# Kernel tuning notes

Measured on AMD Instinct MI355X. Metric: run time of the kernel, lower is better.

The kernel has to match this reference:

```python
import jax, jax.numpy as jnp
import numpy as np


def _topk_masked_softmax(attn, k):
    # Keep only the top-k entries per row (last dim), softmax over them.
    _, idx = jax.lax.top_k(attn, k)  # [b, nh, C, k]
    mask = jnp.put_along_axis(
        jnp.zeros(attn.shape, dtype=bool), idx, True, axis=-1, inplace=False
    )
    return jax.nn.softmax(jnp.where(mask, attn, -jnp.inf), axis=-1)


def setup_inputs() -> dict:
    key = jax.random.key(0)
    k0, k1, k2, k3, k4 = jax.random.split(key, 5)
    b, nh, C = 8, 8, 512
    attn = jax.random.normal(k0, (b, nh, C, C), dtype=jnp.float32)
    # In the torch module these are Parameters initialized to 0.2; use random
    # positive scalars of similar scale for a non-degenerate baseline.
    w1 = jax.random.uniform(k1, (1,), dtype=jnp.float32)
    w2 = jax.random.uniform(k2, (1,), dtype=jnp.float32)
    w3 = jax.random.uniform(k3, (1,), dtype=jnp.float32)
    w4 = jax.random.uniform(k4, (1,), dtype=jnp.float32)
    return {"attn": attn, "w1": w1, "w2": w2, "w3": w3, "w4": w4}


def reference(attn, w1, w2, w3, w4):
    C = attn.shape[-1]
    a1 = _topk_masked_softmax(attn, int(C / 2))
    a2 = _topk_masked_softmax(attn, int(C * 2 / 3))
    a3 = _topk_masked_softmax(attn, int(C * 3 / 4))
    a4 = _topk_masked_softmax(attn, int(C * 4 / 5))
    return a1 * w1 + a2 * w2 + a3 * w3 + a4 * w4
```

## Files before the change

### kernel.cpp

```cpp
#include <hip/hip_runtime.h>
#include <math.h>

#define ROW_C 512
#define NBIN 2048
#define NPACK (NBIN / 2)


static __device__ __forceinline__ unsigned scan64_add(unsigned v) {
    int x = (int)v;
    x += __builtin_amdgcn_update_dpp(0, x, 0x111, 0xF, 0xF, false);
    x += __builtin_amdgcn_update_dpp(0, x, 0x112, 0xF, 0xF, false);
    x += __builtin_amdgcn_update_dpp(0, x, 0x114, 0xF, 0xE, false);
    x += __builtin_amdgcn_update_dpp(0, x, 0x118, 0xF, 0xC, false);
    x += __builtin_amdgcn_update_dpp(0, x, 0x142, 0xA, 0xF, false);
    x += __builtin_amdgcn_update_dpp(0, x, 0x143, 0xC, 0xF, false);
    return (unsigned)x;
}

static __device__ __forceinline__ unsigned scan16_add(unsigned v) {
    int x = (int)v;
    x += __builtin_amdgcn_update_dpp(0, x, 0x111, 0xF, 0xF, false);
    x += __builtin_amdgcn_update_dpp(0, x, 0x112, 0xF, 0xF, false);
    x += __builtin_amdgcn_update_dpp(0, x, 0x114, 0xF, 0xE, false);
    x += __builtin_amdgcn_update_dpp(0, x, 0x118, 0xF, 0xC, false);
    return (unsigned)x;
}

static __device__ __forceinline__ float wave_fadd_red(float v) {
    float t;
    t = __int_as_float(__builtin_amdgcn_update_dpp(0, __float_as_int(v), 0x111, 0xF, 0xF, false)); v += t;
    t = __int_as_float(__builtin_amdgcn_update_dpp(0, __float_as_int(v), 0x112, 0xF, 0xF, false)); v += t;
    t = __int_as_float(__builtin_amdgcn_update_dpp(0, __float_as_int(v), 0x114, 0xF, 0xE, false)); v += t;
    t = __int_as_float(__builtin_amdgcn_update_dpp(0, __float_as_int(v), 0x118, 0xF, 0xC, false)); v += t;
    t = __int_as_float(__builtin_amdgcn_update_dpp(0, __float_as_int(v), 0x142, 0xA, 0xF, false)); v += t;
    t = __int_as_float(__builtin_amdgcn_update_dpp(0, __float_as_int(v), 0x143, 0xC, 0xF, false)); v += t;
    return __int_as_float(__builtin_amdgcn_readlane(__float_as_int(v), 63));
}

static __device__ __forceinline__ float wave_fmax_red(float v) {
    const int NI = (int)0xFF800000;
    float t;
    t = __int_as_float(__builtin_amdgcn_update_dpp(NI, __float_as_int(v), 0x111, 0xF, 0xF, false)); v = fmaxf(v, t);
    t = __int_as_float(__builtin_amdgcn_update_dpp(NI, __float_as_int(v), 0x112, 0xF, 0xF, false)); v = fmaxf(v, t);
    t = __int_as_float(__builtin_amdgcn_update_dpp(NI, __float_as_int(v), 0x114, 0xF, 0xE, false)); v = fmaxf(v, t);
    t = __int_as_float(__builtin_amdgcn_update_dpp(NI, __float_as_int(v), 0x118, 0xF, 0xC, false)); v = fmaxf(v, t);
    t = __int_as_float(__builtin_amdgcn_update_dpp(NI, __float_as_int(v), 0x142, 0xA, 0xF, false)); v = fmaxf(v, t);
    t = __int_as_float(__builtin_amdgcn_update_dpp(NI, __float_as_int(v), 0x143, 0xC, 0xF, false)); v = fmaxf(v, t);
    return __int_as_float(__builtin_amdgcn_readlane(__float_as_int(v), 63));
}

__global__ __launch_bounds__(256) void topk_ms_kernel(
    const float* __restrict__ attn,
    const float* __restrict__ w1p, const float* __restrict__ w2p,
    const float* __restrict__ w3p, const float* __restrict__ w4p,
    float* __restrict__ out)
{
    __shared__ __align__(16) unsigned hist_all[4][NPACK];

    const int lane = threadIdx.x & 63;
    const int wv   = threadIdx.x >> 6;
    unsigned* h = hist_all[wv];
    int4* hv = (int4*)h;

    const long long gid   = (long long)blockIdx.x * 4 + wv;
    const long long baseA = gid * (2 * ROW_C) + lane * 8;
    const long long baseB = baseA + ROW_C;

    float xA[8], xB[8];
    {
        const float4 A0 = *reinterpret_cast<const float4*>(attn + baseA);
        const float4 A1 = *reinterpret_cast<const float4*>(attn + baseA + 4);
        const float4 B0 = *reinterpret_cast<const float4*>(attn + baseB);
        const float4 B1 = *reinterpret_cast<const float4*>(attn + baseB + 4);
        xA[0]=A0.x; xA[1]=A0.y; xA[2]=A0.z; xA[3]=A0.w;
        xA[4]=A1.x; xA[5]=A1.y; xA[6]=A1.z; xA[7]=A1.w;
        xB[0]=B0.x; xB[1]=B0.y; xB[2]=B0.z; xB[3]=B0.w;
        xB[4]=B1.x; xB[5]=B1.y; xB[6]=B1.z; xB[7]=B1.w;
    }

    const float NINF = -__builtin_inff();

    auto BINF = [](float v) -> int {
        const float y = __builtin_amdgcn_fmed3f(v, -3.90625f, 3.90625f) + 12.0f;
        return (int)((__float_as_uint(y) >> 12) & 0x7FFu);
    };

    auto ZERO = [&]() {
        const int4 z = make_int4(0, 0, 0, 0);
        hv[lane] = z; hv[lane + 64] = z; hv[lane + 128] = z; hv[lane + 192] = z;
    };

    auto HIST = [&](const float* x) {
        #pragma unroll
        for (int s = 0; s < 8; ++s) {
            const int b  = BINF(x[s]);
            const int j  = b >> 1;
            const int ph = j ^ ((j >> 3) & 0x1C);
            atomicAdd(&h[ph], (b & 1) ? 0x10000u : 1u);
        }
    };

    auto FRONT = [&](float* tthr, int* b_, int* R_, int* al_) {
        unsigned ps = 0;
        #pragma unroll
        for (int k = 0; k < 4; ++k) {
            const int b  = 4 * lane + k;
            const int pb = b ^ ((b >> 3) & 7);
            const int4 v = hv[pb];
            ps += (unsigned)v.x + (unsigned)v.y + (unsigned)v.z + (unsigned)v.w;
        }
        const unsigned tot  = (ps & 0xFFFFu) + (ps >> 16);
        const unsigned incl = scan64_add(tot);
        const unsigned excl = incl - tot;

        const unsigned long long Ba = __ballot(incl >= 257u);
        const unsigned long long Bb = __ballot(incl >= 172u);
        const unsigned long long Bc = __ballot(incl >= 129u);
        const unsigned long long Bd = __ballot(incl >= 104u);
        const int l0 = __ffsll(Ba) - 1, l1 = __ffsll(Bb) - 1,
                  l2 = __ffsll(Bc) - 1, l3 = __ffsll(Bd) - 1;

        const int r = lane >> 4;
        const int lsel = (r == 0) ? l0 : (r == 1) ? l1 : (r == 2) ? l2 : l3;
        const int Tr   = (r == 0) ? 257 : (r == 1) ? 172 : (r == 2) ? 129 : 104;
        const int Kr   = (r == 0) ? 256 : (r == 1) ? 341 : (r == 2) ? 384 : 409;
        const unsigned exl = __shfl(excl, lsel, 64);

        const int jw = (lsel << 4) + (lane & 15);
        const int pw = jw ^ ((jw >> 3) & 0x1C);
        const unsigned w0 = h[pw];
        const unsigned q  = w0 + (w0 << 16);
        const unsigned wt = q >> 16;
        const unsigned sc = scan16_add(wt);
        const unsigned ebase = exl + (sc - wt);
        const int      phi   = (int)(ebase + wt);
        const unsigned long long CB = __ballot(phi >= Tr);
        const int js = __ffs((unsigned)(CB >> (r << 4))) - 1;
        const unsigned q_w  = __shfl(q, (r << 4) + js, 64);
        const unsigned eb_w = __shfl(ebase, (r << 4) + js, 64);

        const int  plo  = (int)(eb_w + (q_w & 0xFFFFu));
        const int  phw  = (int)(eb_w + (q_w >> 16));
        const bool ev   = (plo >= Tr);
        const int  bsel = (((lsel << 4) + js) << 1) + (ev ? 0 : 1);
        const int  locp = ev ? plo : phw;
        const int  prvp = ev ? (int)eb_w : plo;
        const int  Rr   = Kr - 512 + locp;
        const int  alin = (prvp == Tr - 1) ? 1 : 0;
        const unsigned pk = ((unsigned)bsel << 11) | ((unsigned)alin << 10) | (unsigned)Rr;

        const unsigned v0 = (unsigned)__builtin_amdgcn_readlane((int)pk, 0);
        const unsigned v1 = (unsigned)__builtin_amdgcn_readlane((int)pk, 16);
        const unsigned v2 = (unsigned)__builtin_amdgcn_readlane((int)pk, 32);
        const unsigned v3 = (unsigned)__builtin_amdgcn_readlane((int)pk, 48);
        const unsigned vv[4] = {v0, v1, v2, v3};
        #pragma unroll
        for (int rr = 0; rr < 4; ++rr) {
            b_[rr]  = (int)(vv[rr] >> 11);
            al_[rr] = (int)((vv[rr] >> 10) & 1u);
            R_[rr]  = (int)(vv[rr] & 0x3FFu);
            float t = __uint_as_float((unsigned)(b_[rr] + 0x41000) << 12) - 12.0f;
            tthr[rr] = (b_[rr] <= 24) ? NINF : t;
        }
    };

    auto BACK = [&](const float* x, float* tthr, const int* b_, const int* R_,
                    const int* al_, long long obase) {
        int needv[4] = {0,0,0,0}, cntv[4] = {0,0,0,0};
        bool anytb = false;
        const bool needbins = !(al_[0] && al_[1] && al_[2] && al_[3]);
        int bn[8];
        if (needbins) {
            #pragma unroll
            for (int s = 0; s < 8; ++s) bn[s] = BINF(x[s]);
        }
        #pragma unroll
        for (int rr = 0; rr < 4; ++rr) {
            if (!al_[rr]) {
                float cm[8];
                #pragma unroll
                for (int s = 0; s < 8; ++s)
                    cm[s] = (bn[s] == b_[rr]) ? x[s] : NINF;
                int R = R_[rr];
                float t; int c;
                while (true) {
                    float mk = cm[0];
                    #pragma unroll
                    for (int s = 1; s < 8; ++s) mk = fmaxf(mk, cm[s]);
                    t = wave_fmax_red(mk);
                    c = 0;
                    #pragma unroll
                    for (int s = 0; s < 8; ++s)
                        c += (int)__popcll(__ballot(cm[s] == t));
                    if (c >= R) break;
                    R -= c;
                    #pragma unroll
                    for (int s = 0; s < 8; ++s)
                        cm[s] = (cm[s] == t) ? NINF : cm[s];
                }
                tthr[rr] = t; needv[rr] = R; cntv[rr] = c;
                anytb = anytb || (c != R);
            }
        }

        float eo[8];
        #pragma unroll
        for (int s = 0; s < 8; ++s) eo[s] = __expf(x[s]);

        float res[8];
        if (!anytb) {
            const float t1 = tthr[0], t2 = tthr[1], t3 = tthr[2], t4 = tthr[3];
            float z0 = 0.f, z1 = 0.f, z2 = 0.f, z3 = 0.f;
            #pragma unroll
            for (int s = 0; s < 8; ++s) {
                z0 += (x[s] >= t1) ? eo[s] : 0.f;
                z1 += (x[s] >= t2) ? eo[s] : 0.f;
                z2 += (x[s] >= t3) ? eo[s] : 0.f;
                z3 += (x[s] >= t4) ? eo[s] : 0.f;
            }
            const float Z0 = wave_fadd_red(z0);
            const float Z1 = wave_fadd_red(z1);
            const float Z2 = wave_fadd_red(z2);
            const float Z3 = wave_fadd_red(z3);
            const float wz0 = w1p[0] * __builtin_amdgcn_rcpf(Z0);
            const float wz1 = w2p[0] * __builtin_amdgcn_rcpf(Z1);
            const float wz2 = w3p[0] * __builtin_amdgcn_rcpf(Z2);
            const float wz3 = w4p[0] * __builtin_amdgcn_rcpf(Z3);
            const float u4 = wz3, u3 = u4 + wz2, u2 = u3 + wz1, u1 = u2 + wz0;
            #pragma unroll
            for (int s = 0; s < 8; ++s) {
                float c = (x[s] >= t1) ? u1 : u2;
                c = (x[s] >= t2) ? c : u3;
                c = (x[s] >= t3) ? c : u4;
                c = (x[s] >= t4) ? c : 0.f;
                res[s] = eo[s] * c;
            }
        } else {
            int fl[8] = {0, 0, 0, 0, 0, 0, 0, 0};
            #pragma unroll
            for (int rr = 0; rr < 4; ++rr) {
                const float t = tthr[rr];
                if (al_[rr] || needv[rr] == cntv[rr]) {
                    #pragma unroll
                    for (int s = 0; s < 8; ++s)
                        fl[s] |= ((int)(x[s] >= t)) << rr;
                } else {
                    const unsigned long long ltm = (1ull << lane) - 1ull;
                    int basec = 0;
                    #pragma unroll
                    for (int s = 0; s < 8; ++s)
                        basec += (int)__popcll(__ballot(x[s] == t) & ltm);
                    int own = 0;
                    #pragma unroll
                    for (int s = 0; s < 8; ++s) {
                        const bool eq = (x[s] == t);
                        if (x[s] > t || (eq && (basec + own) < needv[rr]))
                            fl[s] |= (1 << rr);
                        own += eq ? 1 : 0;
                    }
                }
            }
            float z0 = 0.f, z1 = 0.f, z2 = 0.f, z3 = 0.f;
            #pragma unroll
            for (int s = 0; s < 8; ++s) {
                z0 += (fl[s] & 1) ? eo[s] : 0.f;
                z1 += (fl[s] & 2) ? eo[s] : 0.f;
                z2 += (fl[s] & 4) ? eo[s] : 0.f;
                z3 += (fl[s] & 8) ? eo[s] : 0.f;
            }
            const float Z0 = wave_fadd_red(z0);
            const float Z1 = wave_fadd_red(z1);
            const float Z2 = wave_fadd_red(z2);
            const float Z3 = wave_fadd_red(z3);
            const float wz0 = w1p[0] * __builtin_amdgcn_rcpf(Z0);
            const float wz1 = w2p[0] * __builtin_amdgcn_rcpf(Z1);
            const float wz2 = w3p[0] * __builtin_amdgcn_rcpf(Z2);
            const float wz3 = w4p[0] * __builtin_amdgcn_rcpf(Z3);
            #pragma unroll
            for (int s = 0; s < 8; ++s) {
                float c = 0.f;
                c += (fl[s] & 1) ? wz0 : 0.f;
                c += (fl[s] & 2) ? wz1 : 0.f;
                c += (fl[s] & 4) ? wz2 : 0.f;
                c += (fl[s] & 8) ? wz3 : 0.f;
                res[s] = eo[s] * c;
            }
        }

        *reinterpret_cast<float4*>(out + obase)     = make_float4(res[0], res[1], res[2], res[3]);
        *reinterpret_cast<float4*>(out + obase + 4) = make_float4(res[4], res[5], res[6], res[7]);
    };

    ZERO();
    HIST(xA);
    float tthrA[4]; int bA[4], RA[4], alA[4];
    FRONT(tthrA, bA, RA, alA);

    ZERO();
    HIST(xB);

    BACK(xA, tthrA, bA, RA, alA, baseA);
    float tthrB[4]; int bB[4], RB[4], alB[4];
    FRONT(tthrB, bB, RB, alB);
    BACK(xB, tthrB, bB, RB, alB, baseB);
}

extern "C" void kernel_launch(void* const* d_in, const int* in_sizes, int n_in,
                              void* d_out, int out_size, void* d_ws, size_t ws_size,
                              hipStream_t stream) {
    const float* attn = (const float*)d_in[0];
    const float* w1   = (const float*)d_in[1];
    const float* w2   = (const float*)d_in[2];
    const float* w3   = (const float*)d_in[3];
    const float* w4   = (const float*)d_in[4];
    float* out = (float*)d_out;

    int rows  = in_sizes[0] / ROW_C;
    int waves = rows / 2;
    int blocks = (waves + 3) / 4;
    topk_ms_kernel<<<blocks, 256, 0, stream>>>(attn, w1, w2, w3, w4, out);
}
```

Baseline: 123.4 us.

## Process four rows per wave with software-pipelined prefetch and histogram

Each wave now handles four rows instead of two. The next row's load and histogram are interleaved with the current row's front and back phases, so memory latency is hidden and the setup cost is spread over more rows. The front phase replaces cross-lane shuffles with scalar readlanes computed per threshold, and the weight scalars are hoisted out of the loop, with launch bounds set to request 8 blocks. Halving the grid size reduces parallelism, so less latency is hidden across waves on a large GPU.

```diff
diff --git a/kernel.cpp b/kernel.cpp
--- a/kernel.cpp
+++ b/kernel.cpp
@@ -4,6 +4,7 @@
 #define ROW_C 512
 #define NBIN 2048
 #define NPACK (NBIN / 2)
+#define RPW 4
 
 
 static __device__ __forceinline__ unsigned scan64_add(unsigned v) {
@@ -49,7 +50,7 @@
     return __int_as_float(__builtin_amdgcn_readlane(__float_as_int(v), 63));
 }
 
-__global__ __launch_bounds__(256) void topk_ms_kernel(
+__global__ __launch_bounds__(256, 8) void topk_ms_kernel(
     const float* __restrict__ attn,
     const float* __restrict__ w1p, const float* __restrict__ w2p,
     const float* __restrict__ w3p, const float* __restrict__ w4p,
@@ -62,23 +63,11 @@
     unsigned* h = hist_all[wv];
     int4* hv = (int4*)h;
 
+    const float W1 = w1p[0], W2 = w2p[0], W3 = w3p[0], W4 = w4p[0];
+    const float NINF = -__builtin_inff();
+
     const long long gid   = (long long)blockIdx.x * 4 + wv;
-    const long long baseA = gid * (2 * ROW_C) + lane * 8;
-    const long long baseB = baseA + ROW_C;
-
-    float xA[8], xB[8];
-    {
-        const float4 A0 = *reinterpret_cast<const float4*>(attn + baseA);
-        const float4 A1 = *reinterpret_cast<const float4*>(attn + baseA + 4);
-        const float4 B0 = *reinterpret_cast<const float4*>(attn + baseB);
-        const float4 B1 = *reinterpret_cast<const float4*>(attn + baseB + 4);
-        xA[0]=A0.x; xA[1]=A0.y; xA[2]=A0.z; xA[3]=A0.w;
-        xA[4]=A1.x; xA[5]=A1.y; xA[6]=A1.z; xA[7]=A1.w;
-        xB[0]=B0.x; xB[1]=B0.y; xB[2]=B0.z; xB[3]=B0.w;
-        xB[4]=B1.x; xB[5]=B1.y; xB[6]=B1.z; xB[7]=B1.w;
-    }
-
-    const float NINF = -__builtin_inff();
+    const long long base0 = gid * (RPW * ROW_C) + lane * 8;
 
     auto BINF = [](float v) -> int {
         const float y = __builtin_amdgcn_fmed3f(v, -3.90625f, 3.90625f) + 12.0f;
@@ -120,11 +109,15 @@
         const int l0 = __ffsll(Ba) - 1, l1 = __ffsll(Bb) - 1,
                   l2 = __ffsll(Bc) - 1, l3 = __ffsll(Bd) - 1;
 
+        const unsigned e0 = (unsigned)__builtin_amdgcn_readlane((int)excl, l0);
+        const unsigned e1 = (unsigned)__builtin_amdgcn_readlane((int)excl, l1);
+        const unsigned e2 = (unsigned)__builtin_amdgcn_readlane((int)excl, l2);
+        const unsigned e3 = (unsigned)__builtin_amdgcn_readlane((int)excl, l3);
+
         const int r = lane >> 4;
         const int lsel = (r == 0) ? l0 : (r == 1) ? l1 : (r == 2) ? l2 : l3;
         const int Tr   = (r == 0) ? 257 : (r == 1) ? 172 : (r == 2) ? 129 : 104;
-        const int Kr   = (r == 0) ? 256 : (r == 1) ? 341 : (r == 2) ? 384 : 409;
-        const unsigned exl = __shfl(excl, lsel, 64);
+        const unsigned exl = (r == 0) ? e0 : (r == 1) ? e1 : (r == 2) ? e2 : e3;
 
         const int jw = (lsel << 4) + (lane & 15);
         const int pw = jw ^ ((jw >> 3) & 0x1C);
@@ -135,32 +128,28 @@
         const unsigned ebase = exl + (sc - wt);
         const int      phi   = (int)(ebase + wt);
         const unsigned long long CB = __ballot(phi >= Tr);
-        const int js = __ffs((unsigned)(CB >> (r << 4))) - 1;
-        const unsigned q_w  = __shfl(q, (r << 4) + js, 64);
-        const unsigned eb_w = __shfl(ebase, (r << 4) + js, 64);
-
-        const int  plo  = (int)(eb_w + (q_w & 0xFFFFu));
-        const int  phw  = (int)(eb_w + (q_w >> 16));
-        const bool ev   = (plo >= Tr);
-        const int  bsel = (((lsel << 4) + js) << 1) + (ev ? 0 : 1);
-        const int  locp = ev ? plo : phw;
-        const int  prvp = ev ? (int)eb_w : plo;
-        const int  Rr   = Kr - 512 + locp;
-        const int  alin = (prvp == Tr - 1) ? 1 : 0;
-        const unsigned pk = ((unsigned)bsel << 11) | ((unsigned)alin << 10) | (unsigned)Rr;
-
-        const unsigned v0 = (unsigned)__builtin_amdgcn_readlane((int)pk, 0);
-        const unsigned v1 = (unsigned)__builtin_amdgcn_readlane((int)pk, 16);
-        const unsigned v2 = (unsigned)__builtin_amdgcn_readlane((int)pk, 32);
-        const unsigned v3 = (unsigned)__builtin_amdgcn_readlane((int)pk, 48);
-        const unsigned vv[4] = {v0, v1, v2, v3};
+
+        const int Ls[4] = {l0, l1, l2, l3};
+        const int Ts[4] = {257, 172, 129, 104};
+        const int Ks[4] = {256, 341, 384, 409};
         #pragma unroll
         for (int rr = 0; rr < 4; ++rr) {
-            b_[rr]  = (int)(vv[rr] >> 11);
-            al_[rr] = (int)((vv[rr] >> 10) & 1u);
-            R_[rr]  = (int)(vv[rr] & 0x3FFu);
-            float t = __uint_as_float((unsigned)(b_[rr] + 0x41000) << 12) - 12.0f;
-            tthr[rr] = (b_[rr] <= 24) ? NINF : t;
+            const unsigned cb = (unsigned)(CB >> (rr << 4)) & 0xFFFFu;
+            const int js = __ffs(cb) - 1;
+            const int li = (rr << 4) + js;
+            const unsigned qw  = (unsigned)__builtin_amdgcn_readlane((int)q, li);
+            const unsigned ebw = (unsigned)__builtin_amdgcn_readlane((int)ebase, li);
+            const int  plo  = (int)(ebw + (qw & 0xFFFFu));
+            const int  phw  = (int)(ebw + (qw >> 16));
+            const bool ev   = (plo >= Ts[rr]);
+            const int  bsel = (((Ls[rr] << 4) + js) << 1) + (ev ? 0 : 1);
+            const int  locp = ev ? plo : phw;
+            const int  prvp = ev ? (int)ebw : plo;
+            b_[rr]  = bsel;
+            R_[rr]  = Ks[rr] - 512 + locp;
+            al_[rr] = (prvp == Ts[rr] - 1) ? 1 : 0;
+            const float t = __uint_as_float((unsigned)(bsel + 0x41000) << 12) - 12.0f;
+            tthr[rr] = (bsel <= 24) ? NINF : t;
         }
     };
 
@@ -222,10 +211,10 @@
             const float Z1 = wave_fadd_red(z1);
             const float Z2 = wave_fadd_red(z2);
             const float Z3 = wave_fadd_red(z3);
-            const float wz0 = w1p[0] * __builtin_amdgcn_rcpf(Z0);
-            const float wz1 = w2p[0] * __builtin_amdgcn_rcpf(Z1);
-            const float wz2 = w3p[0] * __builtin_amdgcn_rcpf(Z2);
-            const float wz3 = w4p[0] * __builtin_amdgcn_rcpf(Z3);
+            const float wz0 = W1 * __builtin_amdgcn_rcpf(Z0);
+            const float wz1 = W2 * __builtin_amdgcn_rcpf(Z1);
+            const float wz2 = W3 * __builtin_amdgcn_rcpf(Z2);
+            const float wz3 = W4 * __builtin_amdgcn_rcpf(Z3);
             const float u4 = wz3, u3 = u4 + wz2, u2 = u3 + wz1, u1 = u2 + wz0;
             #pragma unroll
             for (int s = 0; s < 8; ++s) {
@@ -272,10 +261,10 @@
             const float Z1 = wave_fadd_red(z1);
             const float Z2 = wave_fadd_red(z2);
             const float Z3 = wave_fadd_red(z3);
-            const float wz0 = w1p[0] * __builtin_amdgcn_rcpf(Z0);
-            const float wz1 = w2p[0] * __builtin_amdgcn_rcpf(Z1);
-            const float wz2 = w3p[0] * __builtin_amdgcn_rcpf(Z2);
-            const float wz3 = w4p[0] * __builtin_amdgcn_rcpf(Z3);
+            const float wz0 = W1 * __builtin_amdgcn_rcpf(Z0);
+            const float wz1 = W2 * __builtin_amdgcn_rcpf(Z1);
+            const float wz2 = W3 * __builtin_amdgcn_rcpf(Z2);
+            const float wz3 = W4 * __builtin_amdgcn_rcpf(Z3);
             #pragma unroll
             for (int s = 0; s < 8; ++s) {
                 float c = 0.f;
@@ -291,18 +280,35 @@
         *reinterpret_cast<float4*>(out + obase + 4) = make_float4(res[4], res[5], res[6], res[7]);
     };
 
+    float xc[8], xn[8];
+    {
+        const float4 A = *reinterpret_cast<const float4*>(attn + base0);
+        const float4 B = *reinterpret_cast<const float4*>(attn + base0 + 4);
+        xc[0]=A.x; xc[1]=A.y; xc[2]=A.z; xc[3]=A.w;
+        xc[4]=B.x; xc[5]=B.y; xc[6]=B.z; xc[7]=B.w;
+    }
     ZERO();
-    HIST(xA);
-    float tthrA[4]; int bA[4], RA[4], alA[4];
-    FRONT(tthrA, bA, RA, alA);
-
-    ZERO();
-    HIST(xB);
-
-    BACK(xA, tthrA, bA, RA, alA, baseA);
-    float tthrB[4]; int bB[4], RB[4], alB[4];
-    FRONT(tthrB, bB, RB, alB);
-    BACK(xB, tthrB, bB, RB, alB, baseB);
+    HIST(xc);
+
+    #pragma unroll
+    for (int i = 0; i < RPW; ++i) {
+        const long long basei = base0 + (long long)i * ROW_C;
+        if (i + 1 < RPW) {
+            const long long basen = basei + ROW_C;
+            const float4 A = *reinterpret_cast<const float4*>(attn + basen);
+            const float4 B = *reinterpret_cast<const float4*>(attn + basen + 4);
+            xn[0]=A.x; xn[1]=A.y; xn[2]=A.z; xn[3]=A.w;
+            xn[4]=B.x; xn[5]=B.y; xn[6]=B.z; xn[7]=B.w;
+        }
+        float tthr[4]; int b_[4], R_[4], al_[4];
+        FRONT(tthr, b_, R_, al_);
+        if (i + 1 < RPW) { ZERO(); HIST(xn); }
+        BACK(xc, tthr, b_, R_, al_, basei);
+        if (i + 1 < RPW) {
+            #pragma unroll
+            for (int s = 0; s < 8; ++s) xc[s] = xn[s];
+        }
+    }
 }
 
 extern "C" void kernel_launch(void* const* d_in, const int* in_sizes, int n_in,
@@ -315,8 +321,8 @@
     const float* w4   = (const float*)d_in[4];
     float* out = (float*)d_out;
 
-    int rows  = in_sizes[0] / ROW_C;
-    int waves = rows / 2;
+    int rows   = in_sizes[0] / ROW_C;
+    int waves  = rows / RPW;
     int blocks = (waves + 3) / 4;
     topk_ms_kernel<<<blocks, 256, 0, stream>>>(attn, w1, w2, w3, w4, out);
 }
```

New measurement: 134.0 us. 1.09x slower.
